# Optimization experiments

Measured on AMD Instinct MI355X. Metric: run time of the kernel, lower is better.

The kernel has to match this reference:

```python
import jax, jax.numpy as jnp
import numpy as np

ITERS = 3; S = 8; I = 64; E = 64; C = 64; DIN = 128; SLOT = 128; H = 256
B = 64; N = 4096; EPS = 1e-8

def _ln(x, g, b):
    m = jnp.mean(x, -1, keepdims=True)
    v = jnp.var(x, -1, keepdims=True)
    return (x - m) * jax.lax.rsqrt(v + 1e-5) * g + b

def _gru(x, h, Wih, Whh, bih, bhh):
    # torch nn.GRUCell math; W stored as [in, 3*hidden]
    gi = x @ Wih + bih
    gh = h @ Whh + bhh
    ir, iz, inn = jnp.split(gi, 3, -1)
    hr, hz, hn = jnp.split(gh, 3, -1)
    r = jax.nn.sigmoid(ir + hr)
    z = jax.nn.sigmoid(iz + hz)
    n = jnp.tanh(inn + r * hn)
    return (1.0 - z) * n + z * h

def setup_inputs() -> dict:
    k = jax.random.split(jax.random.key(0), 32)
    d = {}
    d['slots_bck'] = jax.random.normal(k[0], (B, 1, SLOT), jnp.float32)
    d['inputs'] = jax.random.normal(k[1], (B, N, DIN), jnp.float32)
    d['protos'] = jax.random.normal(k[2], (C, I), jnp.float32)
    d['ext_noise'] = jax.random.normal(k[3], (B, S, E), jnp.float32)
    d['int_noise'] = jax.random.normal(k[4], (B, S, C), jnp.float32)
    u = jax.random.uniform(k[5], (ITERS, B, S, C), jnp.float32, 1e-6, 1.0 - 1e-6)
    d['gumbel'] = -jnp.log(-jnp.log(u))
    d['tau'] = 1
    w = lambda i, shape, s=0.05: jax.random.normal(k[i], shape, jnp.float32) * s
    d['ext_mu'] = w(6, (1, 1, E)); d['ext_log_sigma'] = w(7, (1, 1, E))
    d['int_mu'] = w(8, (1, 1, C)); d['int_log_sigma'] = w(9, (1, 1, C))
    d['ln_in_g'] = jnp.ones((DIN,)); d['ln_in_b'] = jnp.zeros((DIN,))
    d['ln_p_g'] = jnp.ones((I,)); d['ln_p_b'] = jnp.zeros((I,))
    d['ln_mi_g'] = jnp.ones((I,)); d['ln_mi_b'] = jnp.zeros((I,))
    d['ln_me_g'] = jnp.ones((E,)); d['ln_me_b'] = jnp.zeros((E,))
    d['Wq'] = w(10, (SLOT, SLOT)); d['Wk'] = w(11, (DIN, SLOT))
    d['Wv'] = w(12, (DIN, SLOT)); d['Wp'] = w(13, (I, I))
    d['gi_Wih'] = w(14, (I, 3 * I)); d['gi_Whh'] = w(15, (I, 3 * I))
    d['gi_bih'] = jnp.zeros((3 * I,)); d['gi_bhh'] = jnp.zeros((3 * I,))
    d['ge_Wih'] = w(16, (E, 3 * E)); d['ge_Whh'] = w(17, (E, 3 * E))
    d['ge_bih'] = jnp.zeros((3 * E,)); d['ge_bhh'] = jnp.zeros((3 * E,))
    d['mi_W1'] = w(18, (I, H)); d['mi_b1'] = jnp.zeros((H,))
    d['mi_W2'] = w(19, (H, I)); d['mi_b2'] = jnp.zeros((I,))
    d['me_W1'] = w(20, (E, H)); d['me_b1'] = jnp.zeros((H,))
    d['me_W2'] = w(21, (H, E)); d['me_b2'] = jnp.zeros((E,))
    return d

def reference(slots_bck, inputs, protos, ext_noise, int_noise, gumbel,
              ext_mu, ext_log_sigma, int_mu, int_log_sigma,
              ln_in_g, ln_in_b, ln_p_g, ln_p_b, ln_mi_g, ln_mi_b, ln_me_g, ln_me_b,
              Wq, Wk, Wv, Wp,
              gi_Wih, gi_Whh, gi_bih, gi_bhh, ge_Wih, ge_Whh, ge_bih, ge_bhh,
              mi_W1, mi_b1, mi_W2, mi_b2, me_W1, me_b1, me_W2, me_b2, tau):
    Bsz = inputs.shape[0]
    slots_ext = ext_mu + jnp.exp(ext_log_sigma) * ext_noise            # [B,S,E]
    logits_pi = int_mu + jnp.exp(int_log_sigma) * int_noise            # [B,S,C]
    x = _ln(inputs, ln_in_g, ln_in_b)
    kk = (x @ Wk) * (SLOT ** -0.5)                                     # [B,N,SLOT]
    vv = x @ Wv                                                        # [B,N,SLOT]
    p = _ln(protos, ln_p_g, ln_p_b) @ Wp                               # [C,I]
    attn_vis = None
    for i in range(ITERS):
        pi = jax.nn.softmax((logits_pi + gumbel[i]) / tau, axis=-1)    # soft gumbel-softmax
        slots_int = pi @ p                                             # [B,S,I]
        slots_obj = jnp.concatenate([slots_int, slots_ext], -1)        # [B,S,SLOT]
        slots = jnp.concatenate([slots_bck, slots_obj[:, 1:]], 1)
        q = slots @ Wq                                                 # [B,S,SLOT]
        attn_logits = jnp.einsum('bnd,bsd->bns', kk, q)
        attn_vis = jax.nn.softmax(attn_logits, -1)                     # softmax over slots
        attn = attn_vis + EPS
        attn = attn / jnp.sum(attn, -2, keepdims=True)                 # renorm over inputs
        updates = jnp.einsum('bns,bnd->bsd', attn, vv)                 # [B,S,SLOT]
        upd_int, upd_ext = updates[..., :I], updates[..., I:]
        slots_ext = _gru(upd_ext.reshape(-1, E), slots_ext.reshape(-1, E),
                         ge_Wih, ge_Whh, ge_bih, ge_bhh).reshape(Bsz, S, E)
        if i < ITERS - 1:
            h = _ln(slots_ext, ln_me_g, ln_me_b)
            slots_ext = slots_ext + (jax.nn.relu(h @ me_W1 + me_b1) @ me_W2 + me_b2)
        int_upd = _gru(upd_int.reshape(-1, I), slots_int.reshape(-1, I),
                       gi_Wih, gi_Whh, gi_bih, gi_bhh).reshape(Bsz, S, I)
        if i < ITERS - 1:
            h = _ln(int_upd, ln_mi_g, ln_mi_b)
            int_upd = int_upd + (jax.nn.relu(h @ mi_W1 + mi_b1) @ mi_W2 + mi_b2)
        logits_pi = (int_upd @ p.T) * (I ** -0.5)
    return slots_ext[:, 1:], logits_pi[:, 1:], attn_vis
```

## Files before the change

### kernel.cpp

```cpp
#include <hip/hip_runtime.h>
#include <hip/hip_bf16.h>
#include <stdint.h>

typedef unsigned short u16;
#define DEVFN static __device__ __forceinline__

typedef __attribute__((ext_vector_type(8))) short bf16x8;
typedef __attribute__((ext_vector_type(4))) float f32x4;
typedef __attribute__((ext_vector_type(2))) unsigned int u32x2;

constexpr int   kB   = 64;
constexpr int   kN   = 4096;
constexpr float kEPS = 1e-8f;
constexpr float kLNE = 1e-5f;
constexpr float kKSC = 0.08838834764831845f;
constexpr float kISC = 0.125f;

DEVFN u16 f2bf(float f) {
    union { float f; uint32_t u; } x; x.f = f;
    uint32_t r = (x.u + 0x7fffu + ((x.u >> 16) & 1u)) >> 16;
    return (u16)r;
}
DEVFN uint32_t pk2(float lo, float hi) {
    __hip_bfloat162 h = __float22bfloat162_rn(make_float2(lo, hi));
    uint32_t u; __builtin_memcpy(&u, &h, 4); return u;
}
DEVFN u16 bf1(float f) {
    __hip_bfloat16 h = __float2bfloat16(f);
    u16 u; __builtin_memcpy(&u, &h, 2); return u;
}
DEVFN void nts8(u16* p, uint32_t lo, uint32_t hi) {
    u32x2 v; v[0] = lo; v[1] = hi;
    __builtin_nontemporal_store(v, (u32x2*)p);
}
DEVFN float sigf(float x) { return 1.0f / (1.0f + __expf(-x)); }
DEVFN float read_tau(const void* taup) {
    float inv_tau = 1.0f;
    int iv = *(const int*)taup;
    if (iv > 0 && iv < 1000000) inv_tau = 1.0f / (float)iv;
    else {
        float fv = *(const float*)taup;
        if (fv > 1e-6f && fv < 1e6f) inv_tau = 1.0f / fv;
    }
    return inv_tau;
}

__global__ void ksetup(const float* __restrict__ ext_mu, const float* __restrict__ ext_ls,
                       const float* __restrict__ int_mu, const float* __restrict__ int_ls,
                       const float* __restrict__ ext_noise, const float* __restrict__ int_noise,
                       float* __restrict__ sext, float* __restrict__ lpi,
                       const float* __restrict__ Wk, const float* __restrict__ Wv,
                       u16* __restrict__ WT,
                       const float* __restrict__ protos, const float* __restrict__ Wp,
                       const float* __restrict__ lpg, const float* __restrict__ lpb,
                       float* __restrict__ p, float* __restrict__ pT)
{
    __shared__ float pl[64][65];
    __shared__ float mS[64], sS[64];
    const int blk = blockIdx.x;
    const int t = threadIdx.x;
    if (blk < 128) {
        int idx = blk * 256 + t;
        int e = idx & 63;
        sext[idx] = ext_mu[e] + __expf(ext_ls[e]) * ext_noise[idx];
        lpi[idx]  = int_mu[e] + __expf(int_ls[e]) * int_noise[idx];
        return;
    }
    if (blk < 256) {
        int idx = (blk - 128) * 256 + t;
        int k = idx >> 8, c = idx & 255;
        float v = (c < 128) ? Wk[k * 128 + c] * kKSC : Wv[k * 128 + (c - 128)];
        WT[(size_t)c * 128 + k] = f2bf(v);
        return;
    }
    for (int idx = t; idx < 64 * 64; idx += 256) pl[idx >> 6][idx & 63] = protos[idx];
    __syncthreads();
    if (t < 64) {
        float sm = 0.f, sq = 0.f;
        for (int k = 0; k < 64; ++k) { float v = pl[t][k]; sm += v; sq += v * v; }
        float m = sm * (1.0f / 64.0f);
        float var = sq * (1.0f / 64.0f) - m * m;
        mS[t] = m; sS[t] = rsqrtf(var + kLNE);
    }
    __syncthreads();
    for (int idx = t; idx < 64 * 64; idx += 256) {
        int r = idx >> 6, c = idx & 63;
        pl[r][c] = (pl[r][c] - mS[r]) * sS[r] * lpg[c] + lpb[c];
    }
    __syncthreads();
    for (int idx = t; idx < 64 * 64; idx += 256) {
        int r = idx >> 6, c = idx & 63;
        float acc = 0.f;
        for (int k = 0; k < 64; ++k) acc += pl[r][k] * Wp[k * 64 + c];
        p[r * 64 + c] = acc;
        pT[c * 64 + r] = acc;
    }
}

__global__ __launch_bounds__(256) void kmain(const float* __restrict__ inputs,
                                             const u16* __restrict__ WT,
                                             const float* __restrict__ lng, const float* __restrict__ lnb,
                                             u16* __restrict__ kk, u16* __restrict__ vvT,
                                             float* __restrict__ vpart)
{
    __shared__ u16 At[64 * 128];
    const int t = threadIdx.x;
    const int blk = blockIdx.x;
    const int b = blk >> 6;
    const int n0 = (blk & 63) * 64;
    const float* inp = inputs + ((size_t)(b * kN + n0)) * 128;

    f32x4 xv[8];
    #pragma unroll
    for (int j = 0; j < 8; ++j)
        xv[j] = __builtin_nontemporal_load(((const f32x4*)inp) + t + j * 256);

    float s[8], qq[8];
    #pragma unroll
    for (int j = 0; j < 8; ++j) {
        s[j]  = xv[j][0] + xv[j][1] + xv[j][2] + xv[j][3];
        qq[j] = xv[j][0] * xv[j][0] + xv[j][1] * xv[j][1] + xv[j][2] * xv[j][2] + xv[j][3] * xv[j][3];
    }
    #pragma unroll
    for (int d = 16; d >= 1; d >>= 1) {
        #pragma unroll
        for (int j = 0; j < 8; ++j) {
            s[j]  += __shfl_xor(s[j], d);
            qq[j] += __shfl_xor(qq[j], d);
        }
    }
    const int col4 = t & 31;
    const float4 g4 = ((const float4*)lng)[col4];
    const float4 b4 = ((const float4*)lnb)[col4];
    #pragma unroll
    for (int j = 0; j < 8; ++j) {
        const int row = (t >> 5) + 8 * j;
        const float m   = s[j] * (1.0f / 128.0f);
        const float var = qq[j] * (1.0f / 128.0f) - m * m;
        const float sc  = rsqrtf(var + kLNE);
        uint32_t p0 = pk2((xv[j][0] - m) * sc * g4.x + b4.x, (xv[j][1] - m) * sc * g4.y + b4.y);
        uint32_t p1 = pk2((xv[j][2] - m) * sc * g4.z + b4.z, (xv[j][3] - m) * sc * g4.w + b4.w);
        const int byteoff = row * 256 + (((col4 >> 1) ^ (row & 7)) << 4) + ((col4 & 1) << 3);
        *(uint2*)((char*)At + byteoff) = make_uint2(p0, p1);
    }
    __syncthreads();

    const int w  = t >> 6;
    const int l  = t & 63;
    const int lg = l >> 4;
    const int lr = l & 15;
    const bool iskk = (w < 2);

    f32x4 acc[4][4];
    #pragma unroll
    for (int i = 0; i < 4; ++i)
        #pragma unroll
        for (int j = 0; j < 4; ++j) acc[i][j] = (f32x4){0.f, 0.f, 0.f, 0.f};

    #pragma unroll
    for (int ks = 0; ks < 4; ++ks) {
        bf16x8 wf[4], xf[4];
        #pragma unroll
        for (int i = 0; i < 4; ++i)
            wf[i] = *(const bf16x8*)(WT + (size_t)(w * 64 + 16 * i + lr) * 128 + ks * 32 + lg * 8);
        #pragma unroll
        for (int i = 0; i < 4; ++i) {
            const int r2 = 16 * i + lr;
            const int chunk = (ks * 4 + lg) ^ (r2 & 7);
            xf[i] = *(const bf16x8*)((const char*)At + r2 * 256 + chunk * 16);
        }
        if (iskk) {
            #pragma unroll
            for (int i = 0; i < 4; ++i)
                #pragma unroll
                for (int j = 0; j < 4; ++j)
                    acc[i][j] = __builtin_amdgcn_mfma_f32_16x16x32_bf16(wf[i], xf[j], acc[i][j], 0, 0, 0);
        } else {
            #pragma unroll
            for (int i = 0; i < 4; ++i)
                #pragma unroll
                for (int j = 0; j < 4; ++j)
                    acc[i][j] = __builtin_amdgcn_mfma_f32_16x16x32_bf16(xf[i], wf[j], acc[i][j], 0, 0, 0);
        }
    }

    if (iskk) {
        #pragma unroll
        for (int nn = 0; nn < 4; ++nn) {
            const size_t rb = ((size_t)(b * kN) + n0 + 16 * nn + lr) * 128;
            #pragma unroll
            for (int cm = 0; cm < 4; ++cm) {
                nts8(kk + rb + w * 64 + 16 * cm + lg * 4,
                     pk2(acc[cm][nn][0], acc[cm][nn][1]),
                     pk2(acc[cm][nn][2], acc[cm][nn][3]));
            }
        }
    } else {
        #pragma unroll
        for (int ct = 0; ct < 4; ++ct) {
            const int d = (w - 2) * 64 + 16 * ct + lr;
            const size_t db = ((size_t)b * 128 + d) * (size_t)kN;
            #pragma unroll
            for (int m = 0; m < 4; ++m) {
                nts8(vvT + db + n0 + 16 * m + lg * 4,
                     pk2(acc[m][ct][0], acc[m][ct][1]),
                     pk2(acc[m][ct][2], acc[m][ct][3]));
            }
            float sv = 0.f;
            #pragma unroll
            for (int m = 0; m < 4; ++m)
                #pragma unroll
                for (int r = 0; r < 4; ++r) sv += acc[m][ct][r];
            sv += __shfl_xor(sv, 16);
            sv += __shfl_xor(sv, 32);
            if (lg == 0) __builtin_nontemporal_store(sv, &vpart[(size_t)blk * 128 + d]);
        }
    }
}

__global__ void kslots(const float* __restrict__ lpi, const float* __restrict__ gum,
                       const void* __restrict__ taup,
                       const float* __restrict__ p,
                       const float* __restrict__ sbck, const float* __restrict__ sext,
                       const float* __restrict__ Wq,
                       float* __restrict__ sint, float* __restrict__ q,
                       const float* __restrict__ vpart, float* __restrict__ vvsum)
{
    __shared__ float piL[64];
    __shared__ float sv[128];
    const int bs = blockIdx.x;
    const int t = threadIdx.x;
    if (bs >= 512) {
        int idx = (bs - 512) * 128 + t;
        int b = idx >> 7, c = idx & 127;
        float s = 0.f;
        const float* pp = vpart + (size_t)b * 64 * 128 + c;
        for (int nb = 0; nb < 64; ++nb) s += pp[nb * 128];
        vvsum[idx] = s;
        return;
    }
    const int b = bs >> 3, s = bs & 7;
    const float inv_tau = read_tau(taup);
    if (t < 64) {
        float l = (lpi[bs * 64 + t] + gum[bs * 64 + t]) * inv_tau;
        float m = l;
        #pragma unroll
        for (int d = 32; d >= 1; d >>= 1) m = fmaxf(m, __shfl_xor(m, d));
        float e = __expf(l - m);
        float smv = e;
        #pragma unroll
        for (int d = 32; d >= 1; d >>= 1) smv += __shfl_xor(smv, d);
        piL[t] = e / smv;
    }
    __syncthreads();
    if (t < 64) {
        float acc = 0.f;
        for (int c = 0; c < 64; ++c) acc += piL[c] * p[c * 64 + t];
        sint[bs * 64 + t] = acc;
        if (s == 0) {
            sv[t]      = sbck[b * 128 + t];
            sv[64 + t] = sbck[b * 128 + 64 + t];
        } else {
            sv[t]      = acc;
            sv[64 + t] = sext[bs * 64 + t];
        }
    }
    __syncthreads();
    {
        float acc = 0.f;
        for (int k = 0; k < 128; ++k) acc += sv[k] * Wq[k * 128 + t];
        q[bs * 128 + t] = acc;
    }
}

__global__ __launch_bounds__(256) void kattn(const u16* __restrict__ kk, const u16* __restrict__ vvT,
                                             const float* __restrict__ q,
                                             float* __restrict__ attn_out,
                                             float* __restrict__ pu, float* __restrict__ pcs,
                                             const int wvis)
{
    __shared__ u16 qbf[16][128];
    __shared__ u16 aB[4][16][40];
    __shared__ float pwU[4][8][132];
    __shared__ float csL[4][8];
    const int t = threadIdx.x;
    const int blk = blockIdx.x;
    const int b = blk >> 4;
    const int nb = blk & 15;
    const int w = t >> 6, l = t & 63, lg = l >> 4, lr = l & 15;

    {
        float4 v = ((const float4*)(q + (size_t)b * 1024))[t];
        uint2 pk;
        pk.x = pk2(v.x, v.y);
        pk.y = pk2(v.z, v.w);
        *(uint2*)&qbf[t >> 5][(t & 31) * 4] = pk;
        ((uint32_t*)qbf)[512 + t] = 0u;
        ((uint32_t*)qbf)[768 + (t & 255)] = 0u;
    }
    __syncthreads();

    bf16x8 qf[4];
    #pragma unroll
    for (int ks = 0; ks < 4; ++ks) qf[ks] = *(const bf16x8*)&qbf[lr][ks * 32 + lg * 8];

    f32x4 apv[8];
    #pragma unroll
    for (int dt = 0; dt < 8; ++dt) apv[dt] = (f32x4){0.f, 0.f, 0.f, 0.f};
    float cs0 = 0.f, cs1 = 0.f, cs2 = 0.f, cs3 = 0.f;

    const size_t kkb = (size_t)(b * kN) * 128;
    const size_t vvb = (size_t)b * 128 * (size_t)kN;

    #pragma unroll
    for (int ch = 0; ch < 2; ++ch) {
        const int nbase = nb * 256 + w * 64 + ch * 32;
        #pragma unroll
        for (int c2 = 0; c2 < 2; ++c2) {
            const int n16 = nbase + 16 * c2;
            f32x4 pl = (f32x4){0.f, 0.f, 0.f, 0.f};
            #pragma unroll
            for (int ks = 0; ks < 4; ++ks) {
                bf16x8 bfr = *(const bf16x8*)(kk + kkb + (size_t)(n16 + lr) * 128 + ks * 32 + lg * 8);
                pl = __builtin_amdgcn_mfma_f32_16x16x32_bf16(qf[ks], bfr, pl, 0, 0, 0);
            }
            float m = fmaxf(fmaxf(pl[0], pl[1]), fmaxf(pl[2], pl[3]));
            m = fmaxf(m, __shfl_xor(m, 16));
            float e0 = __expf(pl[0] - m), e1 = __expf(pl[1] - m);
            float e2 = __expf(pl[2] - m), e3 = __expf(pl[3] - m);
            float smv = e0 + e1 + e2 + e3;
            smv += __shfl_xor(smv, 16);
            const float inv = 1.0f / smv;
            const float a0 = e0 * inv, a1 = e1 * inv, a2 = e2 * inv, a3 = e3 * inv;
            if (lg < 2) {
                cs0 += a0; cs1 += a1; cs2 += a2; cs3 += a3;
                if (wvis)
                    *(float4*)(attn_out + ((size_t)(b * kN) + n16 + lr) * 8 + lg * 4) =
                        make_float4(a0, a1, a2, a3);
                const int s0 = lg * 4, nn = 16 * c2 + lr;
                aB[w][s0 + 0][nn] = bf1(a0);
                aB[w][s0 + 1][nn] = bf1(a1);
                aB[w][s0 + 2][nn] = bf1(a2);
                aB[w][s0 + 3][nn] = bf1(a3);
            }
        }
        bf16x8 af = *(const bf16x8*)&aB[w][lr][lg * 8];
        #pragma unroll
        for (int dt = 0; dt < 8; ++dt) {
            bf16x8 vfr = *(const bf16x8*)(vvT + vvb + (size_t)(16 * dt + lr) * kN + nbase + lg * 8);
            apv[dt] = __builtin_amdgcn_mfma_f32_16x16x32_bf16(vfr, af, apv[dt], 0, 0, 0);
        }
    }

    if (lr < 8) {
        #pragma unroll
        for (int dt = 0; dt < 8; ++dt)
            *(float4*)&pwU[w][lr][16 * dt + lg * 4] =
                make_float4(apv[dt][0], apv[dt][1], apv[dt][2], apv[dt][3]);
    }
    #pragma unroll
    for (int d = 8; d >= 1; d >>= 1) {
        cs0 += __shfl_xor(cs0, d); cs1 += __shfl_xor(cs1, d);
        cs2 += __shfl_xor(cs2, d); cs3 += __shfl_xor(cs3, d);
    }
    if (lr == 0 && lg < 2) {
        csL[w][lg * 4 + 0] = cs0; csL[w][lg * 4 + 1] = cs1;
        csL[w][lg * 4 + 2] = cs2; csL[w][lg * 4 + 3] = cs3;
    }
    __syncthreads();
    {
        const int s = t >> 5, dq = t & 31;
        float4 r0 = *(const float4*)&pwU[0][s][dq * 4];
        float4 r1 = *(const float4*)&pwU[1][s][dq * 4];
        float4 r2 = *(const float4*)&pwU[2][s][dq * 4];
        float4 r3 = *(const float4*)&pwU[3][s][dq * 4];
        float4 o;
        o.x = r0.x + r1.x + r2.x + r3.x;
        o.y = r0.y + r1.y + r2.y + r3.y;
        o.z = r0.z + r1.z + r2.z + r3.z;
        o.w = r0.w + r1.w + r2.w + r3.w;
        *(float4*)(pu + (size_t)blk * 1024 + s * 128 + dq * 4) = o;
    }
    if (t < 8) pcs[blk * 8 + t] = csL[0][t] + csL[1][t] + csL[2][t] + csL[3][t];
}

__global__ __launch_bounds__(256) void kupdate(
    const float* __restrict__ pu, const float* __restrict__ pcs,
    const float* __restrict__ vvsum, float* __restrict__ sint,
    float* __restrict__ sext, float* __restrict__ lpi,
    const float* __restrict__ giWih, const float* __restrict__ giWhh,
    const float* __restrict__ gibih, const float* __restrict__ gibhh,
    const float* __restrict__ geWih, const float* __restrict__ geWhh,
    const float* __restrict__ gebih, const float* __restrict__ gebhh,
    const float* __restrict__ miW1, const float* __restrict__ mib1,
    const float* __restrict__ miW2, const float* __restrict__ mib2,
    const float* __restrict__ meW1, const float* __restrict__ meb1,
    const float* __restrict__ meW2, const float* __restrict__ meb2,
    const float* __restrict__ lmig, const float* __restrict__ lmib,
    const float* __restrict__ lmeg, const float* __restrict__ lmeb,
    const float* __restrict__ pT, float* __restrict__ out, const int last,
    const float* __restrict__ gumN, const void* __restrict__ taup,
    const float* __restrict__ p, const float* __restrict__ sbck,
    const float* __restrict__ Wq, float* __restrict__ q)
{
    __shared__ float uL[128], hA[64], hB[64];
    __shared__ float g1[192], g2[192];
    __shared__ float tmp[256];
    __shared__ float outE[64], outI[64];
    __shared__ float lgL[64];
    __shared__ float sv[128];
    const int bs = blockIdx.x;
    const int b = bs >> 3, s = bs & 7;
    const int t = threadIdx.x;

    if (t < 128) {
        float num = 0.f;
        for (int nb = 0; nb < 16; ++nb) num += pu[((size_t)(b * 16 + nb)) * 1024 + s * 128 + t];
        float den = 4096.0f * kEPS;
        for (int nb = 0; nb < 16; ++nb) den += pcs[(b * 16 + nb) * 8 + s];
        uL[t] = (num + kEPS * vvsum[b * 128 + t]) / den;
    } else if (t < 192) {
        hA[t - 128] = sext[bs * 64 + (t - 128)];
    } else {
        hB[t - 192] = sint[bs * 64 + (t - 192)];
    }
    __syncthreads();
    if (t < 192) {
        float a = gebih[t], bb = gebhh[t];
        for (int k = 0; k < 64; ++k) {
            a  = fmaf(uL[64 + k], geWih[k * 192 + t], a);
            bb = fmaf(hA[k],      geWhh[k * 192 + t], bb);
        }
        g1[t] = a; g2[t] = bb;
    }
    __syncthreads();
    if (t < 64) {
        float r = sigf(g1[t] + g2[t]);
        float z = sigf(g1[64 + t] + g2[64 + t]);
        float nn = tanhf(g1[128 + t] + r * g2[128 + t]);
        outE[t] = (1.0f - z) * nn + z * hA[t];
    }
    __syncthreads();
    if (t < 192) {
        float a = gibih[t], bb = gibhh[t];
        for (int k = 0; k < 64; ++k) {
            a  = fmaf(uL[k], giWih[k * 192 + t], a);
            bb = fmaf(hB[k], giWhh[k * 192 + t], bb);
        }
        g1[t] = a; g2[t] = bb;
    }
    __syncthreads();
    if (t < 64) {
        float r = sigf(g1[t] + g2[t]);
        float z = sigf(g1[64 + t] + g2[64 + t]);
        float nn = tanhf(g1[128 + t] + r * g2[128 + t]);
        outI[t] = (1.0f - z) * nn + z * hB[t];
    }
    __syncthreads();
    if (!last) {
        if (t < 64) {
            float v = outE[t];
            float sm = v, sq = v * v;
            #pragma unroll
            for (int d = 32; d >= 1; d >>= 1) { sm += __shfl_xor(sm, d); sq += __shfl_xor(sq, d); }
            float m = sm * (1.0f / 64.0f), var = sq * (1.0f / 64.0f) - m * m;
            g1[t] = (v - m) * rsqrtf(var + kLNE) * lmeg[t] + lmeb[t];
        }
        __syncthreads();
        {
            float a = meb1[t];
            for (int k = 0; k < 64; ++k) a = fmaf(g1[k], meW1[k * 256 + t], a);
            tmp[t] = fmaxf(a, 0.0f);
        }
        __syncthreads();
        if (t < 64) {
            float o = meb2[t];
            for (int j = 0; j < 256; ++j) o = fmaf(tmp[j], meW2[j * 64 + t], o);
            outE[t] += o;
        }
        __syncthreads();
        if (t < 64) {
            float v = outI[t];
            float sm = v, sq = v * v;
            #pragma unroll
            for (int d = 32; d >= 1; d >>= 1) { sm += __shfl_xor(sm, d); sq += __shfl_xor(sq, d); }
            float m = sm * (1.0f / 64.0f), var = sq * (1.0f / 64.0f) - m * m;
            g1[t] = (v - m) * rsqrtf(var + kLNE) * lmig[t] + lmib[t];
        }
        __syncthreads();
        {
            float a = mib1[t];
            for (int k = 0; k < 64; ++k) a = fmaf(g1[k], miW1[k * 256 + t], a);
            tmp[t] = fmaxf(a, 0.0f);
        }
        __syncthreads();
        if (t < 64) {
            float o = mib2[t];
            for (int j = 0; j < 256; ++j) o = fmaf(tmp[j], miW2[j * 64 + t], o);
            outI[t] += o;
        }
        __syncthreads();
    }
    if (t < 64) {
        float lg = 0.f;
        for (int k = 0; k < 64; ++k) lg = fmaf(outI[k], pT[k * 64 + t], lg);
        lg *= kISC;
        lgL[t] = lg;
        if (last) { if (s > 0) out[28672 + (b * 7 + (s - 1)) * 64 + t] = lg; }
    } else if (t < 128) {
        int c = t - 64;
        float v = outE[c];
        sext[bs * 64 + c] = v;
        if (last && s > 0) out[(b * 7 + (s - 1)) * 64 + c] = v;
    }
    if (last) return;

    __syncthreads();
    const float inv_tau = read_tau(taup);
    if (t < 64) {
        float l = (lgL[t] + gumN[bs * 64 + t]) * inv_tau;
        float m = l;
        #pragma unroll
        for (int d = 32; d >= 1; d >>= 1) m = fmaxf(m, __shfl_xor(m, d));
        float e = __expf(l - m);
        float smv = e;
        #pragma unroll
        for (int d = 32; d >= 1; d >>= 1) smv += __shfl_xor(smv, d);
        tmp[t] = e / smv;
    }
    __syncthreads();
    if (t < 64) {
        float acc = 0.f;
        for (int c = 0; c < 64; ++c) acc += tmp[c] * p[c * 64 + t];
        sint[bs * 64 + t] = acc;
        if (s == 0) {
            sv[t]      = sbck[b * 128 + t];
            sv[64 + t] = sbck[b * 128 + 64 + t];
        } else {
            sv[t]      = acc;
            sv[64 + t] = outE[t];
        }
    }
    __syncthreads();
    if (t < 128) {
        float acc = 0.f;
        for (int k = 0; k < 128; ++k) acc += sv[k] * Wq[k * 128 + t];
        q[bs * 128 + t] = acc;
    }
}

extern "C" void kernel_launch(void* const* d_in, const int* in_sizes, int n_in,
                              void* d_out, int out_size, void* d_ws, size_t ws_size,
                              hipStream_t stream)
{
    (void)in_sizes; (void)n_in; (void)out_size; (void)ws_size;
    const float* slots_bck = (const float*)d_in[0];
    const float* inputs    = (const float*)d_in[1];
    const float* protos    = (const float*)d_in[2];
    const float* ext_noise = (const float*)d_in[3];
    const float* int_noise = (const float*)d_in[4];
    const float* gumbel    = (const float*)d_in[5];
    const void*  taup      = d_in[6];
    const float* ext_mu    = (const float*)d_in[7];
    const float* ext_ls    = (const float*)d_in[8];
    const float* int_mu    = (const float*)d_in[9];
    const float* int_ls    = (const float*)d_in[10];
    const float* ln_in_g   = (const float*)d_in[11];
    const float* ln_in_b   = (const float*)d_in[12];
    const float* ln_p_g    = (const float*)d_in[13];
    const float* ln_p_b    = (const float*)d_in[14];
    const float* ln_mi_g   = (const float*)d_in[15];
    const float* ln_mi_b   = (const float*)d_in[16];
    const float* ln_me_g   = (const float*)d_in[17];
    const float* ln_me_b   = (const float*)d_in[18];
    const float* Wq        = (const float*)d_in[19];
    const float* Wk        = (const float*)d_in[20];
    const float* Wv        = (const float*)d_in[21];
    const float* Wp        = (const float*)d_in[22];
    const float* giWih     = (const float*)d_in[23];
    const float* giWhh     = (const float*)d_in[24];
    const float* gibih     = (const float*)d_in[25];
    const float* gibhh     = (const float*)d_in[26];
    const float* geWih     = (const float*)d_in[27];
    const float* geWhh     = (const float*)d_in[28];
    const float* gebih     = (const float*)d_in[29];
    const float* gebhh     = (const float*)d_in[30];
    const float* miW1      = (const float*)d_in[31];
    const float* mib1      = (const float*)d_in[32];
    const float* miW2      = (const float*)d_in[33];
    const float* mib2      = (const float*)d_in[34];
    const float* meW1      = (const float*)d_in[35];
    const float* meb1      = (const float*)d_in[36];
    const float* meW2      = (const float*)d_in[37];
    const float* meb2      = (const float*)d_in[38];
    float* out = (float*)d_out;

    char* ws = (char*)d_ws;
    size_t o = 0;
    auto alloc = [&](size_t bytes) { size_t r = o; o += (bytes + 255) & ~(size_t)255; return r; };
    u16*   kkp   = (u16*)  (ws + alloc((size_t)kB * kN * 128 * 2));
    u16*   vvTp  = (u16*)  (ws + alloc((size_t)kB * kN * 128 * 2));
    u16*   WT    = (u16*)  (ws + alloc(256 * 128 * 2));
    float* vpart = (float*)(ws + alloc((size_t)4096 * 128 * 4));
    float* vvsum = (float*)(ws + alloc(8192 * 4));
    float* pbuf  = (float*)(ws + alloc(4096 * 4));
    float* pT    = (float*)(ws + alloc(4096 * 4));
    float* sext  = (float*)(ws + alloc(32768 * 4));
    float* lpi   = (float*)(ws + alloc(32768 * 4));
    float* sint  = (float*)(ws + alloc(32768 * 4));
    float* q     = (float*)(ws + alloc(65536 * 4));
    float* pu    = (float*)(ws + alloc((size_t)1024 * 1024 * 4));
    float* pcs   = (float*)(ws + alloc(1024 * 8 * 4));

    ksetup<<<257, 256, 0, stream>>>(ext_mu, ext_ls, int_mu, int_ls, ext_noise, int_noise,
                                    sext, lpi, Wk, Wv, WT, protos, Wp, ln_p_g, ln_p_b, pbuf, pT);
    kmain<<<4096, 256, 0, stream>>>(inputs, WT, ln_in_g, ln_in_b, kkp, vvTp, vpart);
    kslots<<<576, 128, 0, stream>>>(lpi, gumbel, taup, pbuf, slots_bck, sext, Wq, sint, q,
                                    vpart, vvsum);

    for (int i = 0; i < 3; ++i) {
        const int last = (i == 2);
        kattn<<<1024, 256, 0, stream>>>(kkp, vvTp, q, out + 57344, pu, pcs, last ? 1 : 0);
        kupdate<<<512, 256, 0, stream>>>(pu, pcs, vvsum, sint, sext, lpi,
                                         giWih, giWhh, gibih, gibhh,
                                         geWih, geWhh, gebih, gebhh,
                                         miW1, mib1, miW2, mib2,
                                         meW1, meb1, meW2, meb2,
                                         ln_mi_g, ln_mi_b, ln_me_g, ln_me_b,
                                         pT, out, last,
                                         gumbel + (size_t)(i + 1 < 3 ? i + 1 : 0) * 32768,
                                         taup, pbuf, slots_bck, Wq, q);
    }
}
```

Before: 286.4 us.

## Fuse first attention iteration into projection kernel and stage kk/vvT through LDS

Moves the slot-query computation ahead of the projection kernel so kmain can compute the first iteration's attention logits, softmax over slots and partial updates directly from the on-chip k/v tiles. This skips one full kattn pass that would reread kk and vvT from global memory. The kk/vvT outputs are also restaged through swizzled LDS so they are written as coalesced 16-byte stores, replacing the scattered 8-byte nontemporal stores. The cost is more LDS and extra work per block, which may lower occupancy. The partial buffers also grow to 64 per batch, so kupdate must reduce over more of them in the first iteration.

After: 280.6 us. 1.02x faster.

```diff
diff --git a/kernel.cpp b/kernel.cpp
--- a/kernel.cpp
+++ b/kernel.cpp
@@ -7,7 +7,6 @@
 
 typedef __attribute__((ext_vector_type(8))) short bf16x8;
 typedef __attribute__((ext_vector_type(4))) float f32x4;
-typedef __attribute__((ext_vector_type(2))) unsigned int u32x2;
 
 constexpr int   kB   = 64;
 constexpr int   kN   = 4096;
@@ -28,10 +27,6 @@
 DEVFN u16 bf1(float f) {
     __hip_bfloat16 h = __float2bfloat16(f);
     u16 u; __builtin_memcpy(&u, &h, 2); return u;
-}
-DEVFN void nts8(u16* p, uint32_t lo, uint32_t hi) {
-    u32x2 v; v[0] = lo; v[1] = hi;
-    __builtin_nontemporal_store(v, (u32x2*)p);
 }
 DEVFN float sigf(float x) { return 1.0f / (1.0f + __expf(-x)); }
 DEVFN float read_tau(const void* taup) {
@@ -97,148 +92,17 @@
     }
 }
 
-__global__ __launch_bounds__(256) void kmain(const float* __restrict__ inputs,
-                                             const u16* __restrict__ WT,
-                                             const float* __restrict__ lng, const float* __restrict__ lnb,
-                                             u16* __restrict__ kk, u16* __restrict__ vvT,
-                                             float* __restrict__ vpart)
-{
-    __shared__ u16 At[64 * 128];
-    const int t = threadIdx.x;
-    const int blk = blockIdx.x;
-    const int b = blk >> 6;
-    const int n0 = (blk & 63) * 64;
-    const float* inp = inputs + ((size_t)(b * kN + n0)) * 128;
-
-    f32x4 xv[8];
-    #pragma unroll
-    for (int j = 0; j < 8; ++j)
-        xv[j] = __builtin_nontemporal_load(((const f32x4*)inp) + t + j * 256);
-
-    float s[8], qq[8];
-    #pragma unroll
-    for (int j = 0; j < 8; ++j) {
-        s[j]  = xv[j][0] + xv[j][1] + xv[j][2] + xv[j][3];
-        qq[j] = xv[j][0] * xv[j][0] + xv[j][1] * xv[j][1] + xv[j][2] * xv[j][2] + xv[j][3] * xv[j][3];
-    }
-    #pragma unroll
-    for (int d = 16; d >= 1; d >>= 1) {
-        #pragma unroll
-        for (int j = 0; j < 8; ++j) {
-            s[j]  += __shfl_xor(s[j], d);
-            qq[j] += __shfl_xor(qq[j], d);
-        }
-    }
-    const int col4 = t & 31;
-    const float4 g4 = ((const float4*)lng)[col4];
-    const float4 b4 = ((const float4*)lnb)[col4];
-    #pragma unroll
-    for (int j = 0; j < 8; ++j) {
-        const int row = (t >> 5) + 8 * j;
-        const float m   = s[j] * (1.0f / 128.0f);
-        const float var = qq[j] * (1.0f / 128.0f) - m * m;
-        const float sc  = rsqrtf(var + kLNE);
-        uint32_t p0 = pk2((xv[j][0] - m) * sc * g4.x + b4.x, (xv[j][1] - m) * sc * g4.y + b4.y);
-        uint32_t p1 = pk2((xv[j][2] - m) * sc * g4.z + b4.z, (xv[j][3] - m) * sc * g4.w + b4.w);
-        const int byteoff = row * 256 + (((col4 >> 1) ^ (row & 7)) << 4) + ((col4 & 1) << 3);
-        *(uint2*)((char*)At + byteoff) = make_uint2(p0, p1);
-    }
-    __syncthreads();
-
-    const int w  = t >> 6;
-    const int l  = t & 63;
-    const int lg = l >> 4;
-    const int lr = l & 15;
-    const bool iskk = (w < 2);
-
-    f32x4 acc[4][4];
-    #pragma unroll
-    for (int i = 0; i < 4; ++i)
-        #pragma unroll
-        for (int j = 0; j < 4; ++j) acc[i][j] = (f32x4){0.f, 0.f, 0.f, 0.f};
-
-    #pragma unroll
-    for (int ks = 0; ks < 4; ++ks) {
-        bf16x8 wf[4], xf[4];
-        #pragma unroll
-        for (int i = 0; i < 4; ++i)
-            wf[i] = *(const bf16x8*)(WT + (size_t)(w * 64 + 16 * i + lr) * 128 + ks * 32 + lg * 8);
-        #pragma unroll
-        for (int i = 0; i < 4; ++i) {
-            const int r2 = 16 * i + lr;
-            const int chunk = (ks * 4 + lg) ^ (r2 & 7);
-            xf[i] = *(const bf16x8*)((const char*)At + r2 * 256 + chunk * 16);
-        }
-        if (iskk) {
-            #pragma unroll
-            for (int i = 0; i < 4; ++i)
-                #pragma unroll
-                for (int j = 0; j < 4; ++j)
-                    acc[i][j] = __builtin_amdgcn_mfma_f32_16x16x32_bf16(wf[i], xf[j], acc[i][j], 0, 0, 0);
-        } else {
-            #pragma unroll
-            for (int i = 0; i < 4; ++i)
-                #pragma unroll
-                for (int j = 0; j < 4; ++j)
-                    acc[i][j] = __builtin_amdgcn_mfma_f32_16x16x32_bf16(xf[i], wf[j], acc[i][j], 0, 0, 0);
-        }
-    }
-
-    if (iskk) {
-        #pragma unroll
-        for (int nn = 0; nn < 4; ++nn) {
-            const size_t rb = ((size_t)(b * kN) + n0 + 16 * nn + lr) * 128;
-            #pragma unroll
-            for (int cm = 0; cm < 4; ++cm) {
-                nts8(kk + rb + w * 64 + 16 * cm + lg * 4,
-                     pk2(acc[cm][nn][0], acc[cm][nn][1]),
-                     pk2(acc[cm][nn][2], acc[cm][nn][3]));
-            }
-        }
-    } else {
-        #pragma unroll
-        for (int ct = 0; ct < 4; ++ct) {
-            const int d = (w - 2) * 64 + 16 * ct + lr;
-            const size_t db = ((size_t)b * 128 + d) * (size_t)kN;
-            #pragma unroll
-            for (int m = 0; m < 4; ++m) {
-                nts8(vvT + db + n0 + 16 * m + lg * 4,
-                     pk2(acc[m][ct][0], acc[m][ct][1]),
-                     pk2(acc[m][ct][2], acc[m][ct][3]));
-            }
-            float sv = 0.f;
-            #pragma unroll
-            for (int m = 0; m < 4; ++m)
-                #pragma unroll
-                for (int r = 0; r < 4; ++r) sv += acc[m][ct][r];
-            sv += __shfl_xor(sv, 16);
-            sv += __shfl_xor(sv, 32);
-            if (lg == 0) __builtin_nontemporal_store(sv, &vpart[(size_t)blk * 128 + d]);
-        }
-    }
-}
-
 __global__ void kslots(const float* __restrict__ lpi, const float* __restrict__ gum,
                        const void* __restrict__ taup,
                        const float* __restrict__ p,
                        const float* __restrict__ sbck, const float* __restrict__ sext,
                        const float* __restrict__ Wq,
-                       float* __restrict__ sint, float* __restrict__ q,
-                       const float* __restrict__ vpart, float* __restrict__ vvsum)
+                       float* __restrict__ sint, float* __restrict__ q)
 {
     __shared__ float piL[64];
     __shared__ float sv[128];
     const int bs = blockIdx.x;
     const int t = threadIdx.x;
-    if (bs >= 512) {
-        int idx = (bs - 512) * 128 + t;
-        int b = idx >> 7, c = idx & 127;
-        float s = 0.f;
-        const float* pp = vpart + (size_t)b * 64 * 128 + c;
-        for (int nb = 0; nb < 64; ++nb) s += pp[nb * 128];
-        vvsum[idx] = s;
-        return;
-    }
     const int b = bs >> 3, s = bs & 7;
     const float inv_tau = read_tau(taup);
     if (t < 64) {
@@ -271,6 +135,252 @@
         for (int k = 0; k < 128; ++k) acc += sv[k] * Wq[k * 128 + t];
         q[bs * 128 + t] = acc;
     }
+}
+
+__global__ __launch_bounds__(256) void kmain(const float* __restrict__ inputs,
+                                             const u16* __restrict__ WT,
+                                             const float* __restrict__ lng, const float* __restrict__ lnb,
+                                             const float* __restrict__ q0,
+                                             u16* __restrict__ kk, u16* __restrict__ vvT,
+                                             float* __restrict__ vpart,
+                                             float* __restrict__ pu, float* __restrict__ pcs)
+{
+    __shared__ u16 At[64 * 128];
+    __shared__ u16 Bt[128 * 64];
+    __shared__ u16 qbf[16 * 128];
+    __shared__ u16 aB[2][16][40];
+    __shared__ float pwU[2][8][132];
+    __shared__ float csL[2][8];
+    const int t = threadIdx.x;
+    const int blk = blockIdx.x;
+    const int b = blk >> 6;
+    const int n0 = (blk & 63) * 64;
+    const float* inp = inputs + ((size_t)(b * kN + n0)) * 128;
+
+    {
+        float4 v = ((const float4*)(q0 + (size_t)b * 1024))[t];
+        uint2 pk;
+        pk.x = pk2(v.x, v.y);
+        pk.y = pk2(v.z, v.w);
+        *(uint2*)&qbf[(t >> 5) * 128 + (t & 31) * 4] = pk;
+        ((uint32_t*)qbf)[512 + t] = 0u;
+        ((uint32_t*)qbf)[768 + t] = 0u;
+    }
+
+    f32x4 xv[8];
+    #pragma unroll
+    for (int j = 0; j < 8; ++j)
+        xv[j] = __builtin_nontemporal_load(((const f32x4*)inp) + t + j * 256);
+
+    float s[8], qq[8];
+    #pragma unroll
+    for (int j = 0; j < 8; ++j) {
+        s[j]  = xv[j][0] + xv[j][1] + xv[j][2] + xv[j][3];
+        qq[j] = xv[j][0] * xv[j][0] + xv[j][1] * xv[j][1] + xv[j][2] * xv[j][2] + xv[j][3] * xv[j][3];
+    }
+    #pragma unroll
+    for (int d = 16; d >= 1; d >>= 1) {
+        #pragma unroll
+        for (int j = 0; j < 8; ++j) {
+            s[j]  += __shfl_xor(s[j], d);
+            qq[j] += __shfl_xor(qq[j], d);
+        }
+    }
+    const int col4 = t & 31;
+    const float4 g4 = ((const float4*)lng)[col4];
+    const float4 b4 = ((const float4*)lnb)[col4];
+    #pragma unroll
+    for (int j = 0; j < 8; ++j) {
+        const int row = (t >> 5) + 8 * j;
+        const float m   = s[j] * (1.0f / 128.0f);
+        const float var = qq[j] * (1.0f / 128.0f) - m * m;
+        const float sc  = rsqrtf(var + kLNE);
+        uint32_t p0 = pk2((xv[j][0] - m) * sc * g4.x + b4.x, (xv[j][1] - m) * sc * g4.y + b4.y);
+        uint32_t p1 = pk2((xv[j][2] - m) * sc * g4.z + b4.z, (xv[j][3] - m) * sc * g4.w + b4.w);
+        const int byteoff = row * 256 + (((col4 >> 1) ^ (row & 7)) << 4) + ((col4 & 1) << 3);
+        *(uint2*)((char*)At + byteoff) = make_uint2(p0, p1);
+    }
+    __syncthreads();
+
+    const int w  = t >> 6;
+    const int l  = t & 63;
+    const int lg = l >> 4;
+    const int lr = l & 15;
+    const bool iskk = (w < 2);
+
+    f32x4 acc[4][4];
+    #pragma unroll
+    for (int i = 0; i < 4; ++i)
+        #pragma unroll
+        for (int j = 0; j < 4; ++j) acc[i][j] = (f32x4){0.f, 0.f, 0.f, 0.f};
+
+    #pragma unroll
+    for (int ks = 0; ks < 4; ++ks) {
+        bf16x8 wf[4], xf[4];
+        #pragma unroll
+        for (int i = 0; i < 4; ++i)
+            wf[i] = *(const bf16x8*)(WT + (size_t)(w * 64 + 16 * i + lr) * 128 + ks * 32 + lg * 8);
+        #pragma unroll
+        for (int i = 0; i < 4; ++i) {
+            const int r2 = 16 * i + lr;
+            const int chunk = (ks * 4 + lg) ^ (r2 & 7);
+            xf[i] = *(const bf16x8*)((const char*)At + r2 * 256 + chunk * 16);
+        }
+        if (iskk) {
+            #pragma unroll
+            for (int i = 0; i < 4; ++i)
+                #pragma unroll
+                for (int j = 0; j < 4; ++j)
+                    acc[i][j] = __builtin_amdgcn_mfma_f32_16x16x32_bf16(wf[i], xf[j], acc[i][j], 0, 0, 0);
+        } else {
+            #pragma unroll
+            for (int i = 0; i < 4; ++i)
+                #pragma unroll
+                for (int j = 0; j < 4; ++j)
+                    acc[i][j] = __builtin_amdgcn_mfma_f32_16x16x32_bf16(xf[i], wf[j], acc[i][j], 0, 0, 0);
+        }
+    }
+
+    __syncthreads();
+
+    if (iskk) {
+        #pragma unroll
+        for (int cm = 0; cm < 4; ++cm) {
+            const int c0 = w * 64 + 16 * cm + lg * 4;
+            #pragma unroll
+            for (int nn = 0; nn < 4; ++nn) {
+                const int row = 16 * nn + lr;
+                uint2 pk;
+                pk.x = pk2(acc[cm][nn][0], acc[cm][nn][1]);
+                pk.y = pk2(acc[cm][nn][2], acc[cm][nn][3]);
+                const int byteoff = row * 256 + ((((c0 * 2) >> 4) ^ (row & 7)) << 4) + ((c0 * 2) & 15);
+                *(uint2*)((char*)At + byteoff) = pk;
+            }
+        }
+    } else {
+        #pragma unroll
+        for (int ct = 0; ct < 4; ++ct) {
+            const int d = (w - 2) * 64 + 16 * ct + lr;
+            #pragma unroll
+            for (int m = 0; m < 4; ++m) {
+                const int nn0 = 16 * m + lg * 4;
+                uint2 pk;
+                pk.x = pk2(acc[m][ct][0], acc[m][ct][1]);
+                pk.y = pk2(acc[m][ct][2], acc[m][ct][3]);
+                const int byteoff = d * 128 + ((((nn0 * 2) >> 4) ^ (d & 7)) << 4) + ((nn0 * 2) & 15);
+                *(uint2*)((char*)Bt + byteoff) = pk;
+            }
+            float sv = 0.f;
+            #pragma unroll
+            for (int m = 0; m < 4; ++m)
+                #pragma unroll
+                for (int r = 0; r < 4; ++r) sv += acc[m][ct][r];
+            sv += __shfl_xor(sv, 16);
+            sv += __shfl_xor(sv, 32);
+            if (lg == 0) __builtin_nontemporal_store(sv, &vpart[(size_t)blk * 128 + d]);
+        }
+    }
+    __syncthreads();
+
+    {
+        const size_t kkbase = ((size_t)(b * kN) + n0) * 128;
+        #pragma unroll
+        for (int j = 0; j < 4; ++j) {
+            const int cid = t + j * 256;
+            const int row = cid >> 4, ci = cid & 15;
+            uint4 v = *(const uint4*)((const char*)At + row * 256 + ((ci ^ (row & 7)) << 4));
+            *(uint4*)(kk + kkbase + row * 128 + ci * 8) = v;
+        }
+        const size_t vvbase = (size_t)b * 128 * (size_t)kN + n0;
+        #pragma unroll
+        for (int j = 0; j < 4; ++j) {
+            const int cid = t + j * 256;
+            const int d = cid >> 3, ci = cid & 7;
+            uint4 v = *(const uint4*)((const char*)Bt + d * 128 + ((ci ^ (d & 7)) << 4));
+            *(uint4*)(vvT + vvbase + (size_t)d * kN + ci * 8) = v;
+        }
+    }
+
+    if (w < 2) {
+        bf16x8 qf[4];
+        #pragma unroll
+        for (int ks = 0; ks < 4; ++ks)
+            qf[ks] = *(const bf16x8*)&qbf[lr * 128 + ks * 32 + lg * 8];
+        f32x4 apv[8];
+        #pragma unroll
+        for (int dt = 0; dt < 8; ++dt) apv[dt] = (f32x4){0.f, 0.f, 0.f, 0.f};
+        float cs0 = 0.f, cs1 = 0.f, cs2 = 0.f, cs3 = 0.f;
+        #pragma unroll
+        for (int c2 = 0; c2 < 2; ++c2) {
+            const int rbase = w * 32 + c2 * 16;
+            f32x4 plg = (f32x4){0.f, 0.f, 0.f, 0.f};
+            #pragma unroll
+            for (int ks = 0; ks < 4; ++ks) {
+                const int row = rbase + lr;
+                const int chunk = (ks * 4 + lg) ^ (row & 7);
+                bf16x8 bfr = *(const bf16x8*)((const char*)At + row * 256 + chunk * 16);
+                plg = __builtin_amdgcn_mfma_f32_16x16x32_bf16(qf[ks], bfr, plg, 0, 0, 0);
+            }
+            float m = fmaxf(fmaxf(plg[0], plg[1]), fmaxf(plg[2], plg[3]));
+            m = fmaxf(m, __shfl_xor(m, 16));
+            float e0 = __expf(plg[0] - m), e1 = __expf(plg[1] - m);
+            float e2 = __expf(plg[2] - m), e3 = __expf(plg[3] - m);
+            float smv = e0 + e1 + e2 + e3;
+            smv += __shfl_xor(smv, 16);
+            const float inv = 1.0f / smv;
+            const float a0 = e0 * inv, a1 = e1 * inv, a2 = e2 * inv, a3 = e3 * inv;
+            if (lg < 2) {
+                cs0 += a0; cs1 += a1; cs2 += a2; cs3 += a3;
+                const int s0 = lg * 4, nn = c2 * 16 + lr;
+                aB[w][s0 + 0][nn] = bf1(a0);
+                aB[w][s0 + 1][nn] = bf1(a1);
+                aB[w][s0 + 2][nn] = bf1(a2);
+                aB[w][s0 + 3][nn] = bf1(a3);
+            }
+        }
+        bf16x8 af = *(const bf16x8*)&aB[w][lr][lg * 8];
+        #pragma unroll
+        for (int dt = 0; dt < 8; ++dt) {
+            const int d = 16 * dt + lr;
+            const int nc = (4 * w + lg) ^ (d & 7);
+            bf16x8 vfr = *(const bf16x8*)((const char*)Bt + d * 128 + nc * 16);
+            apv[dt] = __builtin_amdgcn_mfma_f32_16x16x32_bf16(vfr, af, apv[dt], 0, 0, 0);
+        }
+        if (lr < 8) {
+            #pragma unroll
+            for (int dt = 0; dt < 8; ++dt)
+                *(float4*)&pwU[w][lr][16 * dt + lg * 4] =
+                    make_float4(apv[dt][0], apv[dt][1], apv[dt][2], apv[dt][3]);
+        }
+        #pragma unroll
+        for (int d2 = 8; d2 >= 1; d2 >>= 1) {
+            cs0 += __shfl_xor(cs0, d2); cs1 += __shfl_xor(cs1, d2);
+            cs2 += __shfl_xor(cs2, d2); cs3 += __shfl_xor(cs3, d2);
+        }
+        if (lr == 0 && lg < 2) {
+            csL[w][lg * 4 + 0] = cs0; csL[w][lg * 4 + 1] = cs1;
+            csL[w][lg * 4 + 2] = cs2; csL[w][lg * 4 + 3] = cs3;
+        }
+    }
+    __syncthreads();
+    {
+        const int s2 = t >> 5, dq = t & 31;
+        float4 r0 = *(const float4*)&pwU[0][s2][dq * 4];
+        float4 r1 = *(const float4*)&pwU[1][s2][dq * 4];
+        *(float4*)(pu + (size_t)blk * 1024 + s2 * 128 + dq * 4) =
+            make_float4(r0.x + r1.x, r0.y + r1.y, r0.z + r1.z, r0.w + r1.w);
+    }
+    if (t < 8) pcs[blk * 8 + t] = csL[0][t] + csL[1][t];
+}
+
+__global__ void kvvsum(const float* __restrict__ part, float* __restrict__ vvsum)
+{
+    int t = blockIdx.x * 256 + threadIdx.x;
+    int b = t >> 7, c = t & 127;
+    float s = 0.f;
+    const float* pp = part + (size_t)b * 64 * 128 + c;
+    for (int nb = 0; nb < 64; ++nb) s += pp[nb * 128];
+    vvsum[t] = s;
 }
 
 __global__ __launch_bounds__(256) void kattn(const u16* __restrict__ kk, const u16* __restrict__ vvT,
@@ -385,7 +495,7 @@
 }
 
 __global__ __launch_bounds__(256) void kupdate(
-    const float* __restrict__ pu, const float* __restrict__ pcs,
+    const float* __restrict__ pu, const float* __restrict__ pcs, const int nblk,
     const float* __restrict__ vvsum, float* __restrict__ sint,
     float* __restrict__ sext, float* __restrict__ lpi,
     const float* __restrict__ giWih, const float* __restrict__ giWhh,
@@ -415,9 +525,9 @@
 
     if (t < 128) {
         float num = 0.f;
-        for (int nb = 0; nb < 16; ++nb) num += pu[((size_t)(b * 16 + nb)) * 1024 + s * 128 + t];
+        for (int nb = 0; nb < nblk; ++nb) num += pu[((size_t)(b * nblk + nb)) * 1024 + s * 128 + t];
         float den = 4096.0f * kEPS;
-        for (int nb = 0; nb < 16; ++nb) den += pcs[(b * 16 + nb) * 8 + s];
+        for (int nb = 0; nb < nblk; ++nb) den += pcs[(b * nblk + nb) * 8 + s];
         uL[t] = (num + kEPS * vvsum[b * 128 + t]) / den;
     } else if (t < 192) {
         hA[t - 128] = sext[bs * 64 + (t - 128)];
@@ -609,19 +719,20 @@
     float* lpi   = (float*)(ws + alloc(32768 * 4));
     float* sint  = (float*)(ws + alloc(32768 * 4));
     float* q     = (float*)(ws + alloc(65536 * 4));
-    float* pu    = (float*)(ws + alloc((size_t)1024 * 1024 * 4));
-    float* pcs   = (float*)(ws + alloc(1024 * 8 * 4));
+    float* pu    = (float*)(ws + alloc((size_t)4096 * 1024 * 4));
+    float* pcs   = (float*)(ws + alloc(4096 * 8 * 4));
 
     ksetup<<<257, 256, 0, stream>>>(ext_mu, ext_ls, int_mu, int_ls, ext_noise, int_noise,
                                     sext, lpi, Wk, Wv, WT, protos, Wp, ln_p_g, ln_p_b, pbuf, pT);
-    kmain<<<4096, 256, 0, stream>>>(inputs, WT, ln_in_g, ln_in_b, kkp, vvTp, vpart);
-    kslots<<<576, 128, 0, stream>>>(lpi, gumbel, taup, pbuf, slots_bck, sext, Wq, sint, q,
-                                    vpart, vvsum);
+    kslots<<<512, 128, 0, stream>>>(lpi, gumbel, taup, pbuf, slots_bck, sext, Wq, sint, q);
+    kmain<<<4096, 256, 0, stream>>>(inputs, WT, ln_in_g, ln_in_b, q, kkp, vvTp, vpart, pu, pcs);
+    kvvsum<<<32, 256, 0, stream>>>(vpart, vvsum);
 
     for (int i = 0; i < 3; ++i) {
         const int last = (i == 2);
-        kattn<<<1024, 256, 0, stream>>>(kkp, vvTp, q, out + 57344, pu, pcs, last ? 1 : 0);
-        kupdate<<<512, 256, 0, stream>>>(pu, pcs, vvsum, sint, sext, lpi,
+        if (i > 0)
+            kattn<<<1024, 256, 0, stream>>>(kkp, vvTp, q, out + 57344, pu, pcs, last ? 1 : 0);
+        kupdate<<<512, 256, 0, stream>>>(pu, pcs, (i == 0) ? 64 : 16, vvsum, sint, sext, lpi,
                                          giWih, giWhh, gibih, gibhh,
                                          geWih, geWhh, gebih, gebhh,
                                          miW1, mib1, miW2, mib2,
```
